# Optimization experiments

Hardware: AMD Instinct MI355X
Metric: run time of the kernel (lower is better)

## Reference

```python
import jax, jax.numpy as jnp
import numpy as np

N_NODES = 50000


def _gcn_layer(x, src, dst, W, b, n_nodes):
    # x: [N, Cin] -> linear -> [N, Cout]
    h = x @ W.T + b
    # degree over destination (col) index, including self loops
    deg = jax.ops.segment_sum(jnp.ones(src.shape[0], dtype=x.dtype), dst,
                              num_segments=n_nodes)
    dinv = jnp.where(deg > 0, deg ** -0.5, jnp.zeros((), x.dtype))
    norm = dinv[src] * dinv[dst]                      # [E]
    msg = h[src] * norm[:, None]                      # gather + scale
    return jax.ops.segment_sum(msg, dst, num_segments=n_nodes)  # scatter-add


def setup_inputs() -> dict:
    key = jax.random.key(0)
    k1, k2, k3, k4, k5, k6 = jax.random.split(key, 6)
    num_features = 128
    hidden_dim = 128
    n_edges = 1_600_000
    x = jax.random.normal(k1, (N_NODES, num_features), dtype=jnp.float32)
    edge_index = jax.random.randint(k2, (2, n_edges), 0, N_NODES, dtype=jnp.int64)
    bound1 = 1.0 / np.sqrt(num_features)
    W1 = jax.random.uniform(k3, (hidden_dim, num_features), jnp.float32, -bound1, bound1)
    b1 = jax.random.uniform(k4, (hidden_dim,), jnp.float32, -bound1, bound1)
    bound2 = 1.0 / np.sqrt(hidden_dim)
    W2 = jax.random.uniform(k5, (hidden_dim, hidden_dim), jnp.float32, -bound2, bound2)
    b2 = jax.random.uniform(k6, (hidden_dim,), jnp.float32, -bound2, bound2)
    return {"x": x, "edge_index": edge_index, "W1": W1, "b1": b1, "W2": W2, "b2": b2}


def reference(x, edge_index, W1, b1, W2, b2):
    n_nodes = x.shape[0]
    # add_self_loops: append (i, i) for every node
    loops = jnp.arange(n_nodes, dtype=edge_index.dtype)
    src = jnp.concatenate([edge_index[0], loops])
    dst = jnp.concatenate([edge_index[1], loops])
    h = _gcn_layer(x, src, dst, W1, b1, n_nodes)
    h = jax.nn.relu(h)
    # dropout is identity in eval mode (deterministic reference)
    out = _gcn_layer(h, src, dst, W2, b2, n_nodes)
    return out
```

## Files before the change

kernel.cpp:

```cpp
#include <hip/hip_runtime.h>


static constexpr int F = 128;
static constexpr int NR = 128;
static constexpr int CH = 2048;
static constexpr int CAP = 4608;
static constexpr int RMAX = 512;

typedef __attribute__((ext_vector_type(8))) short bf16x8;
typedef __attribute__((ext_vector_type(4))) float f32x4;
typedef __attribute__((ext_vector_type(4))) unsigned short u16x4;

__device__ __forceinline__ unsigned f2b(float x) {
  unsigned u = __float_as_uint(x);
  return (u + 0x7fffu + ((u >> 16) & 1u)) >> 16;
}
__device__ __forceinline__ float b_lo(unsigned u) {
  return __uint_as_float(u << 16);
}
__device__ __forceinline__ float b_hi(unsigned u) {
  return __uint_as_float(u & 0xffff0000u);
}

__global__ __launch_bounds__(512) void k_part(const int* __restrict__ src,
                                              const int* __restrict__ dst,
                                              int E, int R,
                                              int* __restrict__ gcur,
                                              unsigned* __restrict__ rsorted) {
  __shared__ int h[RMAX];
  __shared__ int cur[RMAX];
  const int tid = threadIdx.x;
  for (int i = tid; i < R; i += 512) h[i] = 0;
  __syncthreads();
  const int e0 = blockIdx.x * CH;
  const int idx = e0 + tid * 4;
  int d0 = -1, d1 = -1, d2 = -1, d3 = -1;
  int s0 = 0, s1 = 0, s2 = 0, s3 = 0;
  if (idx + 3 < E) {
    const int4 dv = *(const int4*)(dst + idx);
    const int4 sv = *(const int4*)(src + idx);
    d0 = dv.x; d1 = dv.y; d2 = dv.z; d3 = dv.w;
    s0 = sv.x; s1 = sv.y; s2 = sv.z; s3 = sv.w;
  } else {
    if (idx < E)     { d0 = dst[idx];     s0 = src[idx]; }
    if (idx + 1 < E) { d1 = dst[idx + 1]; s1 = src[idx + 1]; }
    if (idx + 2 < E) { d2 = dst[idx + 2]; s2 = src[idx + 2]; }
    if (idx + 3 < E) { d3 = dst[idx + 3]; s3 = src[idx + 3]; }
  }
  if (d0 >= 0) atomicAdd(&h[d0 >> 7], 1);
  if (d1 >= 0) atomicAdd(&h[d1 >> 7], 1);
  if (d2 >= 0) atomicAdd(&h[d2 >> 7], 1);
  if (d3 >= 0) atomicAdd(&h[d3 >> 7], 1);
  __syncthreads();
  for (int i = tid; i < R; i += 512)
    cur[i] = h[i] ? atomicAdd(&gcur[i], h[i]) : 0;
  __syncthreads();
  if (d0 >= 0) { const int p = atomicAdd(&cur[d0 >> 7], 1); rsorted[p] = ((unsigned)(d0 & (NR - 1)) << 16) | (unsigned)s0; }
  if (d1 >= 0) { const int p = atomicAdd(&cur[d1 >> 7], 1); rsorted[p] = ((unsigned)(d1 & (NR - 1)) << 16) | (unsigned)s1; }
  if (d2 >= 0) { const int p = atomicAdd(&cur[d2 >> 7], 1); rsorted[p] = ((unsigned)(d2 & (NR - 1)) << 16) | (unsigned)s2; }
  if (d3 >= 0) { const int p = atomicAdd(&cur[d3 >> 7], 1); rsorted[p] = ((unsigned)(d3 & (NR - 1)) << 16) | (unsigned)s3; }
}

__global__ __launch_bounds__(512) void k_fillR(
    const unsigned* __restrict__ rsorted, const int* __restrict__ gcur,
    int N, int* __restrict__ rowptr, int* __restrict__ rowend,
    float* __restrict__ dinv, unsigned short* __restrict__ csr) {
  __shared__ unsigned seg[CAP];
  __shared__ int cnt[NR];
  __shared__ int sc[NR];
  __shared__ int cur[NR];
  const int r = blockIdx.x;
  const int tid = threadIdx.x;
  const int b = r * CAP;
  int e = gcur[r];
  if (e > b + CAP) e = b + CAP;
  const int len = e - b;

  if (tid < NR) cnt[tid] = 0;
  __syncthreads();
  for (int i = tid; i < len; i += 512) {
    const unsigned v = rsorted[b + i];
    seg[i] = v;
    atomicAdd(&cnt[v >> 16], 1);
  }
  __syncthreads();
  if (tid < NR) sc[tid] = cnt[tid];
  __syncthreads();
#pragma unroll
  for (int off = 1; off < NR; off <<= 1) {
    const int a = (tid < NR && tid >= off) ? sc[tid - off] : 0;
    __syncthreads();
    if (tid < NR) sc[tid] += a;
    __syncthreads();
  }
  if (tid < NR) {
    const int excl = sc[tid] - cnt[tid];
    cur[tid] = excl;
    const int node = r * NR + tid;
    if (node < N) {
      rowptr[node] = b + excl;
      rowend[node] = b + excl + cnt[tid];
      dinv[node] = rsqrtf((float)(cnt[tid] + 1));
    }
  }
  __syncthreads();
  for (int i = tid; i < len; i += 512) {
    const unsigned v = seg[i];
    const int p = atomicAdd(&cur[v >> 16], 1);
    csr[b + p] = (unsigned short)(v & 0xFFFFu);
  }
}

__global__ __launch_bounds__(256) void k_splitW(
    const float* __restrict__ W1, const float* __restrict__ W2,
    unsigned short* __restrict__ hi1, unsigned short* __restrict__ lo1,
    unsigned short* __restrict__ hi2, unsigned short* __restrict__ lo2,
    int* __restrict__ gcur, int R) {
  const int bi = blockIdx.x;
  const int gi = bi * 256 + threadIdx.x;
  if (gi < R) gcur[gi] = gi * CAP;
  const float* __restrict__ W = (bi < 64) ? W1 : W2;
  unsigned short* __restrict__ hi = (bi < 64) ? hi1 : hi2;
  unsigned short* __restrict__ lo = (bi < 64) ? lo1 : lo2;
  const int i = (bi & 63) * 256 + threadIdx.x;
  const int j = i & 7;
  const int lane = (i >> 3) & 63;
  const int f = (i >> 9) & 7;
  const int t = i >> 12;
  const int col = f * 16 + (lane & 15);
  const int k = t * 32 + ((j & 4) << 2) + 4 * (lane >> 4) + (j & 3);
  const float x = W[col * F + k];
  const unsigned h = f2b(x);
  hi[i] = (unsigned short)h;
  lo[i] = (unsigned short)f2b(x - __uint_as_float(h << 16));
}

template <bool PRESPLIT>
__global__ __launch_bounds__(256) void k_gemm_mfma(
    const float* __restrict__ Af32, const unsigned short* __restrict__ Ahi,
    const unsigned short* __restrict__ Alo,
    const unsigned short* __restrict__ Whi, const unsigned short* __restrict__ Wlo,
    const float* __restrict__ bias, const float* __restrict__ dinv,
    unsigned short* __restrict__ hout, int n, int nTiles) {
  __shared__ unsigned short sWhi[16384];
  __shared__ unsigned short sWlo[16384];
  const int tid = threadIdx.x;
  {
    const uint4* __restrict__ gh = (const uint4*)Whi;
    const uint4* __restrict__ gl = (const uint4*)Wlo;
    uint4* dh = (uint4*)sWhi;
    uint4* dl = (uint4*)sWlo;
#pragma unroll
    for (int i = 0; i < 8; ++i) {
      dh[tid + i * 256] = gh[tid + i * 256];
      dl[tid + i * 256] = gl[tid + i * 256];
    }
  }
  __syncthreads();

  const int wid = tid >> 6;
  const int lane = tid & 63;
  const int r = lane & 15;
  const int g = lane >> 4;

  for (int bt = blockIdx.x; bt < nTiles; bt += gridDim.x) {
    const int m0 = bt * 64 + wid * 16;
    const int arow = m0 + r;

    f32x4 acc[8];
#pragma unroll
    for (int f = 0; f < 8; ++f) acc[f] = (f32x4){0.f, 0.f, 0.f, 0.f};

#pragma unroll
    for (int t = 0; t < 4; ++t) {
      const int kt = t * 32;
      bf16x8 ahi = (bf16x8){0, 0, 0, 0, 0, 0, 0, 0};
      bf16x8 alo = (bf16x8){0, 0, 0, 0, 0, 0, 0, 0};
      if (arow < n) {
        if (PRESPLIT) {
          const size_t ab = (size_t)arow * F + kt + 4 * g;
          const u16x4 h0 = *(const u16x4*)(Ahi + ab);
          const u16x4 h1 = *(const u16x4*)(Ahi + ab + 16);
          const u16x4 l0 = *(const u16x4*)(Alo + ab);
          const u16x4 l1 = *(const u16x4*)(Alo + ab + 16);
          ahi[0] = (short)h0[0]; ahi[1] = (short)h0[1]; ahi[2] = (short)h0[2]; ahi[3] = (short)h0[3];
          ahi[4] = (short)h1[0]; ahi[5] = (short)h1[1]; ahi[6] = (short)h1[2]; ahi[7] = (short)h1[3];
          alo[0] = (short)l0[0]; alo[1] = (short)l0[1]; alo[2] = (short)l0[2]; alo[3] = (short)l0[3];
          alo[4] = (short)l1[0]; alo[5] = (short)l1[1]; alo[6] = (short)l1[2]; alo[7] = (short)l1[3];
        } else {
          const float4 a0 = *(const float4*)(Af32 + (size_t)arow * F + kt + 4 * g);
          const float4 a1 = *(const float4*)(Af32 + (size_t)arow * F + kt + 16 + 4 * g);
          unsigned h;
          h = f2b(a0.x); ahi[0] = (short)h; alo[0] = (short)f2b(a0.x - __uint_as_float(h << 16));
          h = f2b(a0.y); ahi[1] = (short)h; alo[1] = (short)f2b(a0.y - __uint_as_float(h << 16));
          h = f2b(a0.z); ahi[2] = (short)h; alo[2] = (short)f2b(a0.z - __uint_as_float(h << 16));
          h = f2b(a0.w); ahi[3] = (short)h; alo[3] = (short)f2b(a0.w - __uint_as_float(h << 16));
          h = f2b(a1.x); ahi[4] = (short)h; alo[4] = (short)f2b(a1.x - __uint_as_float(h << 16));
          h = f2b(a1.y); ahi[5] = (short)h; alo[5] = (short)f2b(a1.y - __uint_as_float(h << 16));
          h = f2b(a1.z); ahi[6] = (short)h; alo[6] = (short)f2b(a1.z - __uint_as_float(h << 16));
          h = f2b(a1.w); ahi[7] = (short)h; alo[7] = (short)f2b(a1.w - __uint_as_float(h << 16));
        }
      }
#pragma unroll
      for (int f = 0; f < 8; ++f) {
        const bf16x8 bhi = *(const bf16x8*)(sWhi + ((t * 8 + f) * 64 + lane) * 8);
        const bf16x8 blo = *(const bf16x8*)(sWlo + ((t * 8 + f) * 64 + lane) * 8);
        acc[f] = __builtin_amdgcn_mfma_f32_16x16x32_bf16(ahi, bhi, acc[f], 0, 0, 0);
        acc[f] = __builtin_amdgcn_mfma_f32_16x16x32_bf16(ahi, blo, acc[f], 0, 0, 0);
        acc[f] = __builtin_amdgcn_mfma_f32_16x16x32_bf16(alo, bhi, acc[f], 0, 0, 0);
      }
    }

    int orow[4];
    float dv[4];
#pragma unroll
    for (int j = 0; j < 4; ++j) {
      orow[j] = m0 + 4 * g + j;
      dv[j] = (orow[j] < n) ? dinv[orow[j]] : 0.f;
    }
#pragma unroll
    for (int f = 0; f < 8; ++f) {
      const int col = f * 16 + r;
      const float bv = bias[col];
#pragma unroll
      for (int j = 0; j < 4; ++j) {
        if (orow[j] < n)
          hout[(size_t)orow[j] * F + col] = (unsigned short)f2b((acc[f][j] + bv) * dv[j]);
      }
    }
  }
}

template <int MODE>
__global__ __launch_bounds__(256) void k_pull(
    const int* __restrict__ rowptr, const int* __restrict__ rowend,
    const unsigned short* __restrict__ csr, const uint2* __restrict__ h,
    const float* __restrict__ dinv, unsigned short* __restrict__ ahi,
    unsigned short* __restrict__ alo, float* __restrict__ fout, int n) {
  const int wid = (blockIdx.x * blockDim.x + threadIdx.x) >> 6;
  if (wid >= n) return;
  const int lane = threadIdx.x & 63;
  const int half = lane >> 5;
  const int l32 = lane & 31;
  const int beg = rowptr[wid];
  const int end = rowend[wid];

  float4 acc = make_float4(0.f, 0.f, 0.f, 0.f);
  if (half == 0) {
    const uint2 u = h[(size_t)wid * 32 + l32];
    acc.x = b_lo(u.x); acc.y = b_hi(u.x);
    acc.z = b_lo(u.y); acc.w = b_hi(u.y);
  }

  int k = beg + half;
  for (; k + 6 < end; k += 8) {
    const int s0 = csr[k];
    const int s1 = csr[k + 2];
    const int s2 = csr[k + 4];
    const int s3 = csr[k + 6];
    const uint2 u0 = h[(size_t)s0 * 32 + l32];
    const uint2 u1 = h[(size_t)s1 * 32 + l32];
    const uint2 u2 = h[(size_t)s2 * 32 + l32];
    const uint2 u3 = h[(size_t)s3 * 32 + l32];
    acc.x += b_lo(u0.x) + b_lo(u1.x) + b_lo(u2.x) + b_lo(u3.x);
    acc.y += b_hi(u0.x) + b_hi(u1.x) + b_hi(u2.x) + b_hi(u3.x);
    acc.z += b_lo(u0.y) + b_lo(u1.y) + b_lo(u2.y) + b_lo(u3.y);
    acc.w += b_hi(u0.y) + b_hi(u1.y) + b_hi(u2.y) + b_hi(u3.y);
  }
  for (; k < end; k += 2) {
    const uint2 u = h[(size_t)csr[k] * 32 + l32];
    acc.x += b_lo(u.x);
    acc.y += b_hi(u.x);
    acc.z += b_lo(u.y);
    acc.w += b_hi(u.y);
  }

  acc.x += __shfl_xor(acc.x, 32, 64);
  acc.y += __shfl_xor(acc.y, 32, 64);
  acc.z += __shfl_xor(acc.z, 32, 64);
  acc.w += __shfl_xor(acc.w, 32, 64);

  if (half == 0) {
    const float dv = dinv[wid];
    float rx = acc.x * dv;
    float ry = acc.y * dv;
    float rz = acc.z * dv;
    float rw = acc.w * dv;
    if (MODE == 0) {
      rx = fmaxf(rx, 0.f);
      ry = fmaxf(ry, 0.f);
      rz = fmaxf(rz, 0.f);
      rw = fmaxf(rw, 0.f);
      u16x4 hv, lv;
      unsigned u;
      u = f2b(rx); hv[0] = (unsigned short)u; lv[0] = (unsigned short)f2b(rx - __uint_as_float(u << 16));
      u = f2b(ry); hv[1] = (unsigned short)u; lv[1] = (unsigned short)f2b(ry - __uint_as_float(u << 16));
      u = f2b(rz); hv[2] = (unsigned short)u; lv[2] = (unsigned short)f2b(rz - __uint_as_float(u << 16));
      u = f2b(rw); hv[3] = (unsigned short)u; lv[3] = (unsigned short)f2b(rw - __uint_as_float(u << 16));
      *(u16x4*)(ahi + (size_t)wid * F + l32 * 4) = hv;
      *(u16x4*)(alo + (size_t)wid * F + l32 * 4) = lv;
    } else {
      float4 rv;
      rv.x = rx; rv.y = ry; rv.z = rz; rv.w = rw;
      *(float4*)(fout + (size_t)wid * F + l32 * 4) = rv;
    }
  }
}

extern "C" void kernel_launch(void* const* d_in, const int* in_sizes, int n_in,
                              void* d_out, int out_size, void* d_ws, size_t ws_size,
                              hipStream_t stream) {
  const float* x  = (const float*)d_in[0];
  const int*   ei = (const int*)d_in[1];
  const float* W1 = (const float*)d_in[2];
  const float* b1 = (const float*)d_in[3];
  const float* W2 = (const float*)d_in[4];
  const float* b2 = (const float*)d_in[5];

  const int N = in_sizes[0] / F;
  const int E = in_sizes[1] / 2;
  const int* src = ei;
  const int* dst = ei + E;
  const int R = (N + NR - 1) / NR;
  const int C = (E + CH - 1) / CH;

  char* ws = (char*)d_ws;
  int*            gcur    = (int*)(ws + (8u << 10));
  float*          dinv    = (float*)(ws + (16u << 10));
  int*            rowptr  = (int*)(ws + (256u << 10));
  int*            rowend  = (int*)(ws + (512u << 10));
  unsigned short* Whi1    = (unsigned short*)(ws + (768u << 10));
  unsigned short* Wlo1    = (unsigned short*)(ws + (800u << 10));
  unsigned short* Whi2    = (unsigned short*)(ws + (832u << 10));
  unsigned short* Wlo2    = (unsigned short*)(ws + (864u << 10));
  unsigned*       rsorted = (unsigned*)(ws + (1u << 20));
  unsigned short* csr     = (unsigned short*)(ws + (9u << 20));
  unsigned short* hbuf    = (unsigned short*)(ws + (16u << 20));
  unsigned short* Ahi     = (unsigned short*)(ws + (32u << 20));
  unsigned short* Alo     = (unsigned short*)(ws + (45u << 20));
  float*          out     = (float*)d_out;

  const int B = 256;
  const int nTiles = (N + 63) / 64;
  const int gemmBlocks = 512;
  const int pullBlocks = (N * 64 + B - 1) / B;

  k_splitW<<<128, B, 0, stream>>>(W1, W2, Whi1, Wlo1, Whi2, Wlo2, gcur, R);
  k_part<<<C, 512, 0, stream>>>(src, dst, E, R, gcur, rsorted);
  k_fillR<<<R, 512, 0, stream>>>(rsorted, gcur, N, rowptr, rowend, dinv, csr);

  k_gemm_mfma<false><<<gemmBlocks, B, 0, stream>>>(x, nullptr, nullptr, Whi1,
                                                   Wlo1, b1, dinv, hbuf, N,
                                                   nTiles);
  k_pull<0><<<pullBlocks, B, 0, stream>>>(rowptr, rowend, csr,
                                          (const uint2*)hbuf, dinv, Ahi, Alo,
                                          nullptr, N);

  k_gemm_mfma<true><<<gemmBlocks, B, 0, stream>>>(nullptr, Ahi, Alo, Whi2,
                                                  Wlo2, b2, dinv, hbuf, N,
                                                  nTiles);
  k_pull<1><<<pullBlocks, B, 0, stream>>>(rowptr, rowend, csr,
                                          (const uint2*)hbuf, dinv, nullptr,
                                          nullptr, out, N);
}
```

Baseline: 214.3 us.

## Keep split weights in registers and share row tiles across waves

The GEMM kernel no longer stages the split bf16 weight matrices in LDS. Each wave instead loads its own 32-column slice of W hi/lo into registers once, and the four waves of a block split the output columns of one 16-row tile. Tiles shrink to 16 rows and the grid grows to 1024 blocks. This removes the LDS fill, the barrier and the per-iteration LDS reads, and it cuts shared-memory use so more blocks can be resident. In exchange every wave reloads and re-converts the same A rows, so A traffic and conversion work rise about fourfold, and register pressure goes up.

After: 201.3 us. -6.1%, faster.

```diff
diff --git a/kernel.cpp b/kernel.cpp
--- a/kernel.cpp
+++ b/kernel.cpp
@@ -142,34 +142,34 @@
     const unsigned short* __restrict__ Whi, const unsigned short* __restrict__ Wlo,
     const float* __restrict__ bias, const float* __restrict__ dinv,
     unsigned short* __restrict__ hout, int n, int nTiles) {
-  __shared__ unsigned short sWhi[16384];
-  __shared__ unsigned short sWlo[16384];
   const int tid = threadIdx.x;
-  {
-    const uint4* __restrict__ gh = (const uint4*)Whi;
-    const uint4* __restrict__ gl = (const uint4*)Wlo;
-    uint4* dh = (uint4*)sWhi;
-    uint4* dl = (uint4*)sWlo;
-#pragma unroll
-    for (int i = 0; i < 8; ++i) {
-      dh[tid + i * 256] = gh[tid + i * 256];
-      dl[tid + i * 256] = gl[tid + i * 256];
-    }
-  }
-  __syncthreads();
-
   const int wid = tid >> 6;
   const int lane = tid & 63;
   const int r = lane & 15;
   const int g = lane >> 4;
+  const int f0 = 2 * wid;
+
+  bf16x8 bhi[8], blo[8];
+#pragma unroll
+  for (int t = 0; t < 4; ++t) {
+#pragma unroll
+    for (int q = 0; q < 2; ++q) {
+      const size_t base = (((size_t)t * 8 + f0 + q) * 64 + lane) * 8;
+      bhi[t * 2 + q] = *(const bf16x8*)(Whi + base);
+      blo[t * 2 + q] = *(const bf16x8*)(Wlo + base);
+    }
+  }
+  const int col0 = f0 * 16 + r;
+  const int col1 = col0 + 16;
+  const float bv0 = bias[col0];
+  const float bv1 = bias[col1];
 
   for (int bt = blockIdx.x; bt < nTiles; bt += gridDim.x) {
-    const int m0 = bt * 64 + wid * 16;
+    const int m0 = bt * 16;
     const int arow = m0 + r;
 
-    f32x4 acc[8];
-#pragma unroll
-    for (int f = 0; f < 8; ++f) acc[f] = (f32x4){0.f, 0.f, 0.f, 0.f};
+    f32x4 acc0 = (f32x4){0.f, 0.f, 0.f, 0.f};
+    f32x4 acc1 = (f32x4){0.f, 0.f, 0.f, 0.f};
 
 #pragma unroll
     for (int t = 0; t < 4; ++t) {
@@ -201,31 +201,21 @@
           h = f2b(a1.w); ahi[7] = (short)h; alo[7] = (short)f2b(a1.w - __uint_as_float(h << 16));
         }
       }
-#pragma unroll
-      for (int f = 0; f < 8; ++f) {
-        const bf16x8 bhi = *(const bf16x8*)(sWhi + ((t * 8 + f) * 64 + lane) * 8);
-        const bf16x8 blo = *(const bf16x8*)(sWlo + ((t * 8 + f) * 64 + lane) * 8);
-        acc[f] = __builtin_amdgcn_mfma_f32_16x16x32_bf16(ahi, bhi, acc[f], 0, 0, 0);
-        acc[f] = __builtin_amdgcn_mfma_f32_16x16x32_bf16(ahi, blo, acc[f], 0, 0, 0);
-        acc[f] = __builtin_amdgcn_mfma_f32_16x16x32_bf16(alo, bhi, acc[f], 0, 0, 0);
-      }
-    }
-
-    int orow[4];
-    float dv[4];
+      acc0 = __builtin_amdgcn_mfma_f32_16x16x32_bf16(ahi, bhi[t * 2], acc0, 0, 0, 0);
+      acc0 = __builtin_amdgcn_mfma_f32_16x16x32_bf16(ahi, blo[t * 2], acc0, 0, 0, 0);
+      acc0 = __builtin_amdgcn_mfma_f32_16x16x32_bf16(alo, bhi[t * 2], acc0, 0, 0, 0);
+      acc1 = __builtin_amdgcn_mfma_f32_16x16x32_bf16(ahi, bhi[t * 2 + 1], acc1, 0, 0, 0);
+      acc1 = __builtin_amdgcn_mfma_f32_16x16x32_bf16(ahi, blo[t * 2 + 1], acc1, 0, 0, 0);
+      acc1 = __builtin_amdgcn_mfma_f32_16x16x32_bf16(alo, bhi[t * 2 + 1], acc1, 0, 0, 0);
+    }
+
 #pragma unroll
     for (int j = 0; j < 4; ++j) {
-      orow[j] = m0 + 4 * g + j;
-      dv[j] = (orow[j] < n) ? dinv[orow[j]] : 0.f;
-    }
-#pragma unroll
-    for (int f = 0; f < 8; ++f) {
-      const int col = f * 16 + r;
-      const float bv = bias[col];
-#pragma unroll
-      for (int j = 0; j < 4; ++j) {
-        if (orow[j] < n)
-          hout[(size_t)orow[j] * F + col] = (unsigned short)f2b((acc[f][j] + bv) * dv[j]);
+      const int orow = m0 + 4 * g + j;
+      if (orow < n) {
+        const float dv = dinv[orow];
+        hout[(size_t)orow * F + col0] = (unsigned short)f2b((acc0[j] + bv0) * dv);
+        hout[(size_t)orow * F + col1] = (unsigned short)f2b((acc1[j] + bv1) * dv);
       }
     }
   }
@@ -341,8 +331,8 @@
   float*          out     = (float*)d_out;
 
   const int B = 256;
-  const int nTiles = (N + 63) / 64;
-  const int gemmBlocks = 512;
+  const int nTiles = (N + 15) / 16;
+  const int gemmBlocks = 1024;
   const int pullBlocks = (N * 64 + B - 1) / B;
 
   k_splitW<<<128, B, 0, stream>>>(W1, W2, Whi1, Wlo1, Whi2, Wlo2, gcur, R);
```
